# Kernel optimization log

Hardware: AMD Instinct MI355X
Metric: run time of the kernel (lower is better)

Reference implementation:

```python
import jax, jax.numpy as jnp
import numpy as np

N, E, D = 50000, 800000, 64


def setup_inputs() -> dict:
    key = jax.random.key(0)
    k = jax.random.split(key, 6)
    return {
        "graph_embedding": jax.random.normal(k[0], (N, D), dtype=jnp.float32),
        "W": jax.random.normal(k[1], (D, D), dtype=jnp.float32) * (1.0 / np.sqrt(D)),
        "b": jnp.zeros((D,), dtype=jnp.float32),
        "src": jax.random.randint(k[2], (E,), 0, N),
        "dst": jax.random.randint(k[3], (E,), 0, N),
        "e_feat": jax.random.randint(k[4], (E,), 0, 8),
    }


def _gcn_both(x, src, dst, n, W=None, b=None):
    # DGL GraphConv with norm='both': D_out^{-1/2} gather-sum D_in^{-1/2}, then optional weight.
    ones = jnp.ones((src.shape[0],), x.dtype)
    out_deg = jnp.maximum(jax.ops.segment_sum(ones, src, num_segments=n), 1.0)
    in_deg = jnp.maximum(jax.ops.segment_sum(ones, dst, num_segments=n), 1.0)
    x = x * (out_deg ** -0.5)[:, None]
    agg = jax.ops.segment_sum(x[src], dst, num_segments=n)  # [N, D]
    agg = agg * (in_deg ** -0.5)[:, None]
    if W is not None:
        agg = agg @ W + b
    return agg


def reference(graph_embedding, W, b, src, dst, e_feat):
    n = graph_embedding.shape[0]
    # dropout is identity in eval mode
    h = _gcn_both(graph_embedding, src, dst, n)       # layer 0: weight=False
    h = _gcn_both(h, src, dst, n, W, b)               # layer 1: with weight + bias
    # message: ft + sum of masked copies; all ft0/ft2/ft4/ft6 == ft, so per-edge scale
    e = e_feat.reshape(-1, 1).astype(jnp.float32)     # [E, 1], mirrors e_feat.reshape(-1,1).float()
    coef = (1.0 + (e == 0.0) + (e == 2.0) + (e == 4.0) + (e == 6.0)).astype(h.dtype)
    msg = h[src] * coef                               # [E, D] edge gather + scale
    return jax.ops.segment_sum(msg, dst, num_segments=n)  # scatter-sum to dst
```

## Files before the change

### kernel.cpp

```cpp
#include <hip/hip_runtime.h>

#define DD 64
#define CHUNK_A 4096
#define SRC_MASK 0x1FFFF

__global__ __launch_bounds__(256) void k_pre(const int* __restrict__ src,
                                             const int* __restrict__ dst,
                                             int* __restrict__ M,
                                             int* __restrict__ Msrc, int E) {
    __shared__ int hd[256], hs[256];
    int t = threadIdx.x;
    int bid = blockIdx.x;
    hd[t] = 0; hs[t] = 0;
    __syncthreads();
    int base = bid * CHUNK_A;
#pragma unroll
    for (int k = 0; k < CHUNK_A / 256; ++k) {
        int e = base + t + (k << 8);
        if (e < E) {
            atomicAdd(&hd[dst[e] >> 8], 1);
            atomicAdd(&hs[src[e] >> 8], 1);
        }
    }
    __syncthreads();
    M[bid * 256 + t] = hd[t];
    Msrc[bid * 256 + t] = hs[t];
}

__global__ __launch_bounds__(256) void k_binscan(int* __restrict__ M,
                                                 int* __restrict__ Msrc,
                                                 int* __restrict__ binBase,
                                                 int* __restrict__ binBaseS,
                                                 int* __restrict__ rstart,
                                                 int PB, int n, int E) {
    int t = threadIdx.x;
    int* Mx = (blockIdx.x == 0) ? M : Msrc;
    int* bb = (blockIdx.x == 0) ? binBase : binBaseS;
    int tot = 0;
    for (int p = 0; p < PB; ++p) tot += Mx[p * 256 + t];
    int lane = t & 63, w = t >> 6;
    int inc = tot;
    for (int o = 1; o < 64; o <<= 1) {
        int u = __shfl_up(inc, o);
        if (lane >= o) inc += u;
    }
    __shared__ int wtot[4];
    if (lane == 63) wtot[w] = inc;
    __syncthreads();
    int woff = 0;
    for (int i = 0; i < w; ++i) woff += wtot[i];
    int base = woff + inc - tot;
    bb[t] = base;
    if (t == 255) bb[256] = base + tot;
    if (blockIdx.x == 0 && t == 0) rstart[n] = E;
    int run = base;
#pragma unroll 4
    for (int p = 0; p < PB; ++p) {
        int v = Mx[p * 256 + t];
        Mx[p * 256 + t] = run;
        run += v;
    }
}

__global__ __launch_bounds__(256) void k_scatterA(const int* __restrict__ src,
                                                  const int* __restrict__ dst,
                                                  const int* __restrict__ ef,
                                                  const int* __restrict__ M,
                                                  const int* __restrict__ Msrc,
                                                  int* __restrict__ bucketA,
                                                  unsigned char* __restrict__ bucketS,
                                                  int E) {
    __shared__ int curD[256], curS[256];
    int t = threadIdx.x;
    int p = blockIdx.x;
    curD[t] = M[p * 256 + t];
    curS[t] = Msrc[p * 256 + t];
    __syncthreads();
    int base = p * CHUNK_A;
#pragma unroll
    for (int k = 0; k < CHUNK_A / 256; ++k) {
        int e = base + t + (k << 8);
        if (e < E) {
            int s = src[e], d = dst[e];
            int posD = atomicAdd(&curD[d >> 8], 1);
            bucketA[posD] = s | ((ef[e] & 1) << 17) | ((d & 255) << 18);
            int posS = atomicAdd(&curS[s >> 8], 1);
            bucketS[posS] = (unsigned char)(s & 255);
        }
    }
}

__global__ __launch_bounds__(256) void k_bucket(const int* __restrict__ bucketA,
                                                const unsigned char* __restrict__ bucketS,
                                                const int* __restrict__ binBase,
                                                const int* __restrict__ binBaseS,
                                                int* __restrict__ rstart,
                                                float* __restrict__ iinv,
                                                float* __restrict__ oinv,
                                                int* __restrict__ edges, int n, int NB) {
    __shared__ int cnt[256];
    __shared__ int off[256];
    __shared__ int wtot[4];
    int t = threadIdx.x;
    int b = blockIdx.x;
    if (b < NB) {
        int s0 = binBase[b], s1 = binBase[b + 1];
        cnt[t] = 0;
        __syncthreads();
        for (int i = s0 + t; i < s1; i += 256)
            atomicAdd(&cnt[(bucketA[i] >> 18) & 255], 1);
        __syncthreads();
        int c = cnt[t];
        int lane = t & 63, w = t >> 6;
        int inc = c;
        for (int o = 1; o < 64; o <<= 1) {
            int u = __shfl_up(inc, o);
            if (lane >= o) inc += u;
        }
        if (lane == 63) wtot[w] = inc;
        __syncthreads();
        int woff = 0;
        for (int i = 0; i < w; ++i) woff += wtot[i];
        int excl = woff + inc - c;
        int v = b * 256 + t;
        if (v < n) {
            rstart[v] = s0 + excl;
            iinv[v] = rsqrtf((float)max(c, 1));
        }
        off[t] = excl;
        __syncthreads();
        for (int i = s0 + t; i < s1; i += 256) {
            int r = bucketA[i];
            int cc = (r >> 18) & 255;
            int pos = atomicAdd(&off[cc], 1);
            edges[s0 + pos] = (r & SRC_MASK) | (int)(((unsigned)((r >> 17) & 1)) << 31);
        }
    } else {
        int bs = b - NB;
        int s0 = binBaseS[bs], s1 = binBaseS[bs + 1];
        cnt[t] = 0;
        __syncthreads();
        for (int i = s0 + t; i < s1; i += 256)
            atomicAdd(&cnt[(int)bucketS[i]], 1);
        __syncthreads();
        int v = bs * 256 + t;
        if (v < n) oinv[v] = rsqrtf((float)max(cnt[t], 1));
    }
}

template <int MODE>
__global__ __launch_bounds__(256) void k_gather(const float* __restrict__ x,
                                                const int* __restrict__ edges,
                                                const int* __restrict__ row_start,
                                                const float* __restrict__ oinv,
                                                const float* __restrict__ iinv,
                                                float* __restrict__ y, int n) {
    int wave = (blockIdx.x * 256 + threadIdx.x) >> 6;
    if (wave >= n) return;
    int lane = threadIdx.x & 63;
    int sub = lane >> 4;
    int q = lane & 15;
    int s0 = row_start[wave], s1 = row_start[wave + 1];
    float ax = 0.f, ay = 0.f, az = 0.f, aw = 0.f;
    int i = s0 + sub;
    for (; i + 4 < s1; i += 8) {
        int r0 = edges[i], r1 = edges[i + 4];
        int sa = r0 & SRC_MASK, sb = r1 & SRC_MASK;
        const float4 v0 = *(const float4*)(x + (size_t)sa * DD + q * 4);
        const float4 v1 = *(const float4*)(x + (size_t)sb * DD + q * 4);
        float c0 = 1.0f, c1 = 1.0f;
        if (MODE == 0) { c0 = oinv[sa]; c1 = oinv[sb]; }
        if (MODE == 2) { c0 = (r0 < 0) ? 1.0f : 2.0f; c1 = (r1 < 0) ? 1.0f : 2.0f; }
        ax = fmaf(v0.x, c0, ax); ay = fmaf(v0.y, c0, ay);
        az = fmaf(v0.z, c0, az); aw = fmaf(v0.w, c0, aw);
        ax = fmaf(v1.x, c1, ax); ay = fmaf(v1.y, c1, ay);
        az = fmaf(v1.z, c1, az); aw = fmaf(v1.w, c1, aw);
    }
    if (i < s1) {
        int r0 = edges[i];
        int sa = r0 & SRC_MASK;
        const float4 v0 = *(const float4*)(x + (size_t)sa * DD + q * 4);
        float c0 = 1.0f;
        if (MODE == 0) c0 = oinv[sa];
        if (MODE == 2) c0 = (r0 < 0) ? 1.0f : 2.0f;
        ax = fmaf(v0.x, c0, ax); ay = fmaf(v0.y, c0, ay);
        az = fmaf(v0.z, c0, az); aw = fmaf(v0.w, c0, aw);
    }
    ax += __shfl_xor(ax, 16); ay += __shfl_xor(ay, 16);
    az += __shfl_xor(az, 16); aw += __shfl_xor(aw, 16);
    ax += __shfl_xor(ax, 32); ay += __shfl_xor(ay, 32);
    az += __shfl_xor(az, 32); aw += __shfl_xor(aw, 32);
    if (sub == 0) {
        float post = 1.0f;
        if (MODE == 0) post = iinv[wave] * oinv[wave];
        float4 o = make_float4(ax * post, ay * post, az * post, aw * post);
        *(float4*)(y + (size_t)wave * DD + q * 4) = o;
    }
}

__global__ __launch_bounds__(256) void k_gather_gemm(const float* __restrict__ x,
                                                     const int* __restrict__ edges,
                                                     const int* __restrict__ row_start,
                                                     const float* __restrict__ iinv,
                                                     const float* __restrict__ W,
                                                     const float* __restrict__ b,
                                                     float* __restrict__ h1, int n) {
    __shared__ float Wl[64 * 64];
    __shared__ float bl[64];
    __shared__ float wrow[4][64];
    int tid = threadIdx.x;
    const float4* W4 = (const float4*)W;
    float4* Wl4 = (float4*)Wl;
#pragma unroll
    for (int k = 0; k < 4; ++k) Wl4[tid + k * 256] = W4[tid + k * 256];
    if (tid < 64) bl[tid] = b[tid];

    int wave = (blockIdx.x * 256 + tid) >> 6;
    int lane = tid & 63;
    int sub = lane >> 4;
    int q = lane & 15;
    bool valid = wave < n;
    float ax = 0.f, ay = 0.f, az = 0.f, aw = 0.f;
    if (valid) {
        int s0 = row_start[wave], s1 = row_start[wave + 1];
        int i = s0 + sub;
        for (; i + 4 < s1; i += 8) {
            int sa = edges[i] & SRC_MASK, sb = edges[i + 4] & SRC_MASK;
            const float4 v0 = *(const float4*)(x + (size_t)sa * DD + q * 4);
            const float4 v1 = *(const float4*)(x + (size_t)sb * DD + q * 4);
            ax += v0.x; ay += v0.y; az += v0.z; aw += v0.w;
            ax += v1.x; ay += v1.y; az += v1.z; aw += v1.w;
        }
        if (i < s1) {
            int sa = edges[i] & SRC_MASK;
            const float4 v0 = *(const float4*)(x + (size_t)sa * DD + q * 4);
            ax += v0.x; ay += v0.y; az += v0.z; aw += v0.w;
        }
    }
    ax += __shfl_xor(ax, 16); ay += __shfl_xor(ay, 16);
    az += __shfl_xor(az, 16); aw += __shfl_xor(aw, 16);
    ax += __shfl_xor(ax, 32); ay += __shfl_xor(ay, 32);
    az += __shfl_xor(az, 32); aw += __shfl_xor(aw, 32);
    __syncthreads();
    int wid = tid >> 6;
    if (valid && sub == 0) {
        float post = iinv[wave];
        *(float4*)&wrow[wid][q * 4] =
            make_float4(ax * post, ay * post, az * post, aw * post);
    }
    __syncthreads();
    if (valid) {
        float acc = bl[lane];
#pragma unroll
        for (int k = 0; k < 64; ++k) acc = fmaf(wrow[wid][k], Wl[k * 64 + lane], acc);
        h1[(size_t)wave * DD + lane] = acc;
    }
}

extern "C" void kernel_launch(void* const* d_in, const int* in_sizes, int n_in,
                              void* d_out, int out_size, void* d_ws, size_t ws_size,
                              hipStream_t stream) {
    const float* x   = (const float*)d_in[0];
    const float* W   = (const float*)d_in[1];
    const float* b   = (const float*)d_in[2];
    const int*   src = (const int*)d_in[3];
    const int*   dst = (const int*)d_in[4];
    const int*   ef  = (const int*)d_in[5];
    float* out = (float*)d_out;

    const int n = in_sizes[0] / DD;
    const int E = in_sizes[3];

    const int PB = (E + CHUNK_A - 1) / CHUNK_A;
    const int NB = (n + 255) >> 8;

    char* ws = (char*)d_ws;
    size_t np = ((size_t)n + 255) & ~(size_t)255;
    float* oinv    = (float*)ws; ws += np * 4;
    float* iinv    = (float*)ws; ws += np * 4;
    int*   rstart  = (int*)ws;   ws += (np + 256) * 4;
    int*   binBase = (int*)ws;   ws += 260 * 4;
    int*   binBaseS= (int*)ws;   ws += 260 * 4;
    int*   M       = (int*)ws;   ws += (size_t)PB * 256 * 4;
    int*   Msrc    = (int*)ws;   ws += (size_t)PB * 256 * 4;
    int*   bucketA = (int*)ws;   ws += (size_t)E * 4;
    unsigned char* bucketS = (unsigned char*)ws; ws += ((size_t)E + 255) & ~(size_t)255;
    int*   edges   = (int*)ws;   ws += (size_t)E * 4;
    size_t fbytes = (size_t)n * DD * sizeof(float);
    float* h0  = (float*)ws;    ws += fbytes;
    float* agg = (float*)ws;    ws += fbytes;

    k_pre<<<PB, 256, 0, stream>>>(src, dst, M, Msrc, E);
    k_binscan<<<2, 256, 0, stream>>>(M, Msrc, binBase, binBaseS, rstart, PB, n, E);
    k_scatterA<<<PB, 256, 0, stream>>>(src, dst, ef, M, Msrc, bucketA, bucketS, E);
    k_bucket<<<2 * NB, 256, 0, stream>>>(bucketA, bucketS, binBase, binBaseS,
                                         rstart, iinv, oinv, edges, n, NB);

    int gblocks = (n + 3) / 4;
    k_gather<0><<<gblocks, 256, 0, stream>>>(x, edges, rstart, oinv, iinv, h0, n);
    k_gather_gemm<<<gblocks, 256, 0, stream>>>(h0, edges, rstart, iinv, W, b, agg, n);
    k_gather<2><<<gblocks, 256, 0, stream>>>(agg, edges, rstart, oinv, iinv, out, n);
}
```

Baseline: 256.3 us.

## Split features into column quarters for cache-local gathers and separate GEMM

Transposes node features into four 16-column slabs (pre-scaled by out-degree norm) so each gather pass over one slab has a working set that fits better in cache. The gathers run as a 2D grid over nodes and slabs, using 16 edges per wave with float4 lanes. The fused gather+GEMM is split into a separate gather and a tiled 32-row GEMM kernel. Nontemporal loads and stores are added. This costs an extra transpose pass, an extra kernel launch, and four passes over the edge lists instead of one.

Result: slower. 380.6 us (+48.5%).

```diff
diff --git a/kernel.cpp b/kernel.cpp
--- a/kernel.cpp
+++ b/kernel.cpp
@@ -3,6 +3,8 @@
 #define DD 64
 #define CHUNK_A 4096
 #define SRC_MASK 0x1FFFF
+
+typedef float f32x4 __attribute__((ext_vector_type(4)));
 
 __global__ __launch_bounds__(256) void k_pre(const int* __restrict__ src,
                                              const int* __restrict__ dst,
@@ -148,112 +150,98 @@
     }
 }
 
+__global__ __launch_bounds__(256) void k_xpose(const f32x4* __restrict__ x4,
+                                               const float* __restrict__ oinv,
+                                               f32x4* __restrict__ xq4, int n) {
+    int tid = blockIdx.x * 256 + threadIdx.x;
+    if (tid >= n * 16) return;
+    int v = tid >> 4, c = tid & 15;
+    int q = c >> 2, cl = c & 3;
+    f32x4 val = __builtin_nontemporal_load(&x4[tid]);
+    float s = oinv[v];
+    val *= s;
+    __builtin_nontemporal_store(val, &xq4[((size_t)q * n + v) * 4 + cl]);
+}
+
 template <int MODE>
-__global__ __launch_bounds__(256) void k_gather(const float* __restrict__ x,
-                                                const int* __restrict__ edges,
-                                                const int* __restrict__ row_start,
-                                                const float* __restrict__ oinv,
-                                                const float* __restrict__ iinv,
-                                                float* __restrict__ y, int n) {
-    int wave = (blockIdx.x * 256 + threadIdx.x) >> 6;
-    if (wave >= n) return;
+__global__ __launch_bounds__(256) void k_gatherq(const float* __restrict__ xq,
+                                                 const int* __restrict__ edges,
+                                                 const int* __restrict__ rstart,
+                                                 const float* __restrict__ oinv,
+                                                 const float* __restrict__ iinv,
+                                                 float* __restrict__ y, int n) {
+    int v = blockIdx.x * 4 + (threadIdx.x >> 6);
+    if (v >= n) return;
+    int q = blockIdx.y;
     int lane = threadIdx.x & 63;
-    int sub = lane >> 4;
-    int q = lane & 15;
-    int s0 = row_start[wave], s1 = row_start[wave + 1];
+    int slot = lane >> 2;
+    int cl = lane & 3;
+    int s0 = rstart[v], s1 = rstart[v + 1];
+    const float* xb = xq + (size_t)q * n * 16;
     float ax = 0.f, ay = 0.f, az = 0.f, aw = 0.f;
-    int i = s0 + sub;
-    for (; i + 4 < s1; i += 8) {
-        int r0 = edges[i], r1 = edges[i + 4];
-        int sa = r0 & SRC_MASK, sb = r1 & SRC_MASK;
-        const float4 v0 = *(const float4*)(x + (size_t)sa * DD + q * 4);
-        const float4 v1 = *(const float4*)(x + (size_t)sb * DD + q * 4);
-        float c0 = 1.0f, c1 = 1.0f;
-        if (MODE == 0) { c0 = oinv[sa]; c1 = oinv[sb]; }
-        if (MODE == 2) { c0 = (r0 < 0) ? 1.0f : 2.0f; c1 = (r1 < 0) ? 1.0f : 2.0f; }
-        ax = fmaf(v0.x, c0, ax); ay = fmaf(v0.y, c0, ay);
-        az = fmaf(v0.z, c0, az); aw = fmaf(v0.w, c0, aw);
-        ax = fmaf(v1.x, c1, ax); ay = fmaf(v1.y, c1, ay);
-        az = fmaf(v1.z, c1, az); aw = fmaf(v1.w, c1, aw);
-    }
-    if (i < s1) {
-        int r0 = edges[i];
-        int sa = r0 & SRC_MASK;
-        const float4 v0 = *(const float4*)(x + (size_t)sa * DD + q * 4);
-        float c0 = 1.0f;
-        if (MODE == 0) c0 = oinv[sa];
-        if (MODE == 2) c0 = (r0 < 0) ? 1.0f : 2.0f;
-        ax = fmaf(v0.x, c0, ax); ay = fmaf(v0.y, c0, ay);
-        az = fmaf(v0.z, c0, az); aw = fmaf(v0.w, c0, aw);
-    }
-    ax += __shfl_xor(ax, 16); ay += __shfl_xor(ay, 16);
-    az += __shfl_xor(az, 16); aw += __shfl_xor(aw, 16);
-    ax += __shfl_xor(ax, 32); ay += __shfl_xor(ay, 32);
-    az += __shfl_xor(az, 32); aw += __shfl_xor(aw, 32);
-    if (sub == 0) {
+    for (int i = s0 + slot; i < s1; i += 16) {
+        int rec = __builtin_nontemporal_load(&edges[i]);
+        int s = rec & SRC_MASK;
+        const float4 val = *(const float4*)(xb + s * 16 + cl * 4);
+        float sc = 1.0f;
+        if (MODE == 2) sc = (rec < 0) ? 1.0f : 2.0f;
+        ax = fmaf(val.x, sc, ax); ay = fmaf(val.y, sc, ay);
+        az = fmaf(val.z, sc, az); aw = fmaf(val.w, sc, aw);
+    }
+#pragma unroll
+    for (int o = 4; o < 64; o <<= 1) {
+        ax += __shfl_xor(ax, o); ay += __shfl_xor(ay, o);
+        az += __shfl_xor(az, o); aw += __shfl_xor(aw, o);
+    }
+    if (slot == 0) {
         float post = 1.0f;
-        if (MODE == 0) post = iinv[wave] * oinv[wave];
-        float4 o = make_float4(ax * post, ay * post, az * post, aw * post);
-        *(float4*)(y + (size_t)wave * DD + q * 4) = o;
-    }
-}
-
-__global__ __launch_bounds__(256) void k_gather_gemm(const float* __restrict__ x,
-                                                     const int* __restrict__ edges,
-                                                     const int* __restrict__ row_start,
-                                                     const float* __restrict__ iinv,
-                                                     const float* __restrict__ W,
-                                                     const float* __restrict__ b,
-                                                     float* __restrict__ h1, int n) {
+        if (MODE == 0) post = iinv[v] * oinv[v];
+        if (MODE == 1) post = iinv[v];
+        f32x4 o;
+        o.x = ax * post; o.y = ay * post; o.z = az * post; o.w = aw * post;
+        if (MODE == 2)
+            __builtin_nontemporal_store(o, (f32x4*)(y + (size_t)v * DD + q * 16 + cl * 4));
+        else
+            __builtin_nontemporal_store(o, (f32x4*)(y + ((size_t)q * n + v) * 16 + cl * 4));
+    }
+}
+
+__global__ __launch_bounds__(256) void k_gemm_q(const float* __restrict__ aggq,
+                                                const float* __restrict__ W,
+                                                const float* __restrict__ bias,
+                                                float* __restrict__ h1q, int n) {
     __shared__ float Wl[64 * 64];
+    __shared__ float rows[32][64];
     __shared__ float bl[64];
-    __shared__ float wrow[4][64];
     int tid = threadIdx.x;
-    const float4* W4 = (const float4*)W;
-    float4* Wl4 = (float4*)Wl;
+    const f32x4* W4 = (const f32x4*)W;
+    f32x4* Wl4 = (f32x4*)Wl;
 #pragma unroll
     for (int k = 0; k < 4; ++k) Wl4[tid + k * 256] = W4[tid + k * 256];
-    if (tid < 64) bl[tid] = b[tid];
-
-    int wave = (blockIdx.x * 256 + tid) >> 6;
-    int lane = tid & 63;
-    int sub = lane >> 4;
-    int q = lane & 15;
-    bool valid = wave < n;
-    float ax = 0.f, ay = 0.f, az = 0.f, aw = 0.f;
-    if (valid) {
-        int s0 = row_start[wave], s1 = row_start[wave + 1];
-        int i = s0 + sub;
-        for (; i + 4 < s1; i += 8) {
-            int sa = edges[i] & SRC_MASK, sb = edges[i + 4] & SRC_MASK;
-            const float4 v0 = *(const float4*)(x + (size_t)sa * DD + q * 4);
-            const float4 v1 = *(const float4*)(x + (size_t)sb * DD + q * 4);
-            ax += v0.x; ay += v0.y; az += v0.z; aw += v0.w;
-            ax += v1.x; ay += v1.y; az += v1.z; aw += v1.w;
-        }
-        if (i < s1) {
-            int sa = edges[i] & SRC_MASK;
-            const float4 v0 = *(const float4*)(x + (size_t)sa * DD + q * 4);
-            ax += v0.x; ay += v0.y; az += v0.z; aw += v0.w;
-        }
-    }
-    ax += __shfl_xor(ax, 16); ay += __shfl_xor(ay, 16);
-    az += __shfl_xor(az, 16); aw += __shfl_xor(aw, 16);
-    ax += __shfl_xor(ax, 32); ay += __shfl_xor(ay, 32);
-    az += __shfl_xor(az, 32); aw += __shfl_xor(aw, 32);
-    __syncthreads();
-    int wid = tid >> 6;
-    if (valid && sub == 0) {
-        float post = iinv[wave];
-        *(float4*)&wrow[wid][q * 4] =
-            make_float4(ax * post, ay * post, az * post, aw * post);
-    }
-    __syncthreads();
-    if (valid) {
-        float acc = bl[lane];
-#pragma unroll
-        for (int k = 0; k < 64; ++k) acc = fmaf(wrow[wid][k], Wl[k * 64 + lane], acc);
-        h1[(size_t)wave * DD + lane] = acc;
+    if (tid < 64) bl[tid] = bias[tid];
+    int r0 = blockIdx.x * 32;
+    const f32x4* a4 = (const f32x4*)aggq;
+#pragma unroll
+    for (int j = tid; j < 512; j += 256) {
+        int q = j >> 7, rem = j & 127, r = rem >> 2, cl = rem & 3;
+        int gr = r0 + r;
+        f32x4 val = {0.f, 0.f, 0.f, 0.f};
+        if (gr < n) val = __builtin_nontemporal_load(&a4[((size_t)q * n + gr) * 4 + cl]);
+        *(f32x4*)&rows[r][q * 16 + cl * 4] = val;
+    }
+    __syncthreads();
+    int col = tid & 63;
+    int rg = tid >> 6;
+    float bc = bl[col];
+    int qc = col >> 4, clc = col & 15;
+    for (int rr = 0; rr < 8; ++rr) {
+        int r = rg * 8 + rr;
+        int gr = r0 + r;
+        if (gr >= n) break;
+        float acc = bc;
+#pragma unroll
+        for (int k = 0; k < 64; ++k) acc = fmaf(rows[r][k], Wl[k * 64 + col], acc);
+        __builtin_nontemporal_store(acc, &h1q[((size_t)qc * n + gr) * 16 + clc]);
     }
 }
 
@@ -287,8 +275,10 @@
     unsigned char* bucketS = (unsigned char*)ws; ws += ((size_t)E + 255) & ~(size_t)255;
     int*   edges   = (int*)ws;   ws += (size_t)E * 4;
     size_t fbytes = (size_t)n * DD * sizeof(float);
-    float* h0  = (float*)ws;    ws += fbytes;
-    float* agg = (float*)ws;    ws += fbytes;
+    float* xq   = (float*)ws;    ws += fbytes;
+    float* h0q  = (float*)ws;    ws += fbytes;
+    float* aggq = (float*)ws;    ws += fbytes;
+    float* h1q  = xq;
 
     k_pre<<<PB, 256, 0, stream>>>(src, dst, M, Msrc, E);
     k_binscan<<<2, 256, 0, stream>>>(M, Msrc, binBase, binBaseS, rstart, PB, n, E);
@@ -296,8 +286,12 @@
     k_bucket<<<2 * NB, 256, 0, stream>>>(bucketA, bucketS, binBase, binBaseS,
                                          rstart, iinv, oinv, edges, n, NB);
 
-    int gblocks = (n + 3) / 4;
-    k_gather<0><<<gblocks, 256, 0, stream>>>(x, edges, rstart, oinv, iinv, h0, n);
-    k_gather_gemm<<<gblocks, 256, 0, stream>>>(h0, edges, rstart, iinv, W, b, agg, n);
-    k_gather<2><<<gblocks, 256, 0, stream>>>(agg, edges, rstart, oinv, iinv, out, n);
-}
+    k_xpose<<<(n * 16 + 255) / 256, 256, 0, stream>>>((const f32x4*)x, oinv,
+                                                      (f32x4*)xq, n);
+
+    dim3 ggrid((n + 3) / 4, 4);
+    k_gatherq<0><<<ggrid, 256, 0, stream>>>(xq, edges, rstart, oinv, iinv, h0q, n);
+    k_gatherq<1><<<ggrid, 256, 0, stream>>>(h0q, edges, rstart, oinv, iinv, aggq, n);
+    k_gemm_q<<<(n + 31) / 32, 256, 0, stream>>>(aggq, W, b, h1q, n);
+    k_gatherq<2><<<ggrid, 256, 0, stream>>>(h1q, edges, rstart, oinv, iinv, out, n);
+}
```
